# Kernel tuning notes

Measured on AMD Instinct MI355X. Metric: run time of the kernel, lower is better.

## Reference

```python
import jax, jax.numpy as jnp
import numpy as np

B = 16384          # batch
F_S = 26           # number of sparse features
F_D = 13           # number of dense features
V = 100000         # vocab per sparse feature
D = 64             # latent_dim


def setup_inputs() -> dict:
    key = jax.random.key(0)
    ks = jax.random.split(key, 8)
    sparse_idx = jax.random.randint(ks[0], (B, F_S), 0, V, dtype=jnp.int32)
    dense = jax.random.normal(ks[1], (B, F_D), dtype=jnp.float32)
    # Per-feature embedding tables, stacked: [F_S, V, *]
    emb_lin = jax.random.normal(ks[2], (F_S, V), dtype=jnp.float32) * 0.01      # linear_sparse (dim=1)
    emb_v = jax.random.normal(ks[3], (F_S, V, D), dtype=jnp.float32) * 0.01     # sparse_arch
    lin_dense_W = jax.random.normal(ks[4], (1, F_D), dtype=jnp.float32) * 0.1   # linear_dense
    lin_dense_b = jnp.zeros((1,), dtype=jnp.float32)
    dense_arch_W = jax.random.normal(ks[5], (D, F_D), dtype=jnp.float32) * 0.1  # dense_arch
    dense_arch_b = jnp.zeros((D,), dtype=jnp.float32)
    bias = jnp.zeros((1, 1), dtype=jnp.float32)
    return {
        "sparse_idx": sparse_idx, "dense": dense,
        "emb_lin": emb_lin, "emb_v": emb_v,
        "lin_dense_W": lin_dense_W, "lin_dense_b": lin_dense_b,
        "dense_arch_W": dense_arch_W, "dense_arch_b": dense_arch_b,
        "bias": bias,
    }


def reference(sparse_idx, dense, emb_lin, emb_v, lin_dense_W, lin_dense_b,
              dense_arch_W, dense_arch_b, bias):
    feat_ids = jnp.arange(F_S)[None, :]                       # [1, F_S]
    # ----- first-order term -----
    lin_d = dense @ lin_dense_W.T + lin_dense_b               # [B, 1]
    lin_s = emb_lin[feat_ids, sparse_idx]                     # [B, F_S] gather
    first = lin_d + lin_s.sum(axis=1, keepdims=True)          # [B, 1]
    # ----- second-order (FM) term -----
    v_d = dense @ dense_arch_W.T + dense_arch_b               # [B, D]
    v_s = emb_v[feat_ids, sparse_idx]                         # [B, F_S, D] gather
    vecs = jnp.concatenate([v_d[:, None, :], v_s], axis=1)    # [B, F_S+1, D]
    sum_of_square = jnp.square(vecs.sum(axis=1))              # [B, D]
    square_of_sum = jnp.square(vecs).sum(axis=1)              # [B, D]
    second = 0.5 * (sum_of_square - square_of_sum).sum(axis=1, keepdims=True)
    return first + second + bias                              # [B, 1]
```

## Files before the change

kernel.cpp:

```cpp
#include <hip/hip_runtime.h>

#define B   16384
#define F_S 26
#define F_D 13
#define V   100000
#define D   64

__global__ __launch_bounds__(256) void fm_kernel(
    const int*   __restrict__ sparse_idx,
    const float* __restrict__ dense,
    const float* __restrict__ emb_lin,
    const float* __restrict__ emb_v,
    const float* __restrict__ lin_dense_W,
    const float* __restrict__ lin_dense_b,
    const float* __restrict__ dense_arch_W,
    const float* __restrict__ dense_arch_b,
    const float* __restrict__ bias,
    float*       __restrict__ out)
{
    const int wave = threadIdx.x >> 6;
    const int lane = threadIdx.x & 63;
    const int row  = blockIdx.x * 4 + wave;

    int myidx = 0;
    if (lane < F_S) myidx = sparse_idx[row * F_S + lane];

    float dvals[F_D];
#pragma unroll
    for (int j = 0; j < F_D; ++j) dvals[j] = dense[row * F_D + j];

    float vd = dense_arch_b[lane];
#pragma unroll
    for (int j = 0; j < F_D; ++j)
        vd = fmaf(dense_arch_W[lane * F_D + j], dvals[j], vd);

    float S  = vd;
    float sq = vd * vd;

#pragma unroll
    for (int f = 0; f < F_S; ++f) {
        int idxf = __shfl(myidx, f);
        float val = emb_v[((size_t)f * V + (size_t)idxf) * D + lane];
        S  += val;
        sq  = fmaf(val, val, sq);
    }

    float part = 0.5f * (S * S - sq);
    if (lane < F_D) part = fmaf(dvals[lane], lin_dense_W[lane], part);
    if (lane < F_S) part += emb_lin[lane * V + myidx];

#pragma unroll
    for (int off = 32; off > 0; off >>= 1)
        part += __shfl_xor(part, off);

    if (lane == 0)
        out[row] = part + lin_dense_b[0] + bias[0];
}

extern "C" void kernel_launch(void* const* d_in, const int* in_sizes, int n_in,
                              void* d_out, int out_size, void* d_ws, size_t ws_size,
                              hipStream_t stream) {
    const int*   sparse_idx   = (const int*)  d_in[0];
    const float* dense        = (const float*)d_in[1];
    const float* emb_lin      = (const float*)d_in[2];
    const float* emb_v        = (const float*)d_in[3];
    const float* lin_dense_W  = (const float*)d_in[4];
    const float* lin_dense_b  = (const float*)d_in[5];
    const float* dense_arch_W = (const float*)d_in[6];
    const float* dense_arch_b = (const float*)d_in[7];
    const float* bias         = (const float*)d_in[8];
    float*       out          = (float*)d_out;

    fm_kernel<<<dim3(B / 4), dim3(256), 0, stream>>>(
        sparse_idx, dense, emb_lin, emb_v,
        lin_dense_W, lin_dense_b, dense_arch_W, dense_arch_b, bias, out);
}
```

Baseline: 743.1 us.

## Process four rows per wave with float4 embedding loads and LDS-staged indices

Result: no change. 743.8 us (+0.1%).

```diff
diff --git a/kernel.cpp b/kernel.cpp
--- a/kernel.cpp
+++ b/kernel.cpp
@@ -18,42 +18,71 @@
     const float* __restrict__ bias,
     float*       __restrict__ out)
 {
+    __shared__ int sidx[16 * F_S];
+
+    const int iblock = blockIdx.x * 16 * F_S;
+    sidx[threadIdx.x] = sparse_idx[iblock + threadIdx.x];
+    if (threadIdx.x < 16 * F_S - 256)
+        sidx[256 + threadIdx.x] = sparse_idx[iblock + 256 + threadIdx.x];
+    __syncthreads();
+
     const int wave = threadIdx.x >> 6;
     const int lane = threadIdx.x & 63;
-    const int row  = blockIdx.x * 4 + wave;
-
-    int myidx = 0;
-    if (lane < F_S) myidx = sparse_idx[row * F_S + lane];
+    const int sub  = lane >> 4;
+    const int t    = lane & 15;
+    const int rowl = wave * 4 + sub;
+    const int row  = blockIdx.x * 16 + rowl;
 
     float dvals[F_D];
 #pragma unroll
     for (int j = 0; j < F_D; ++j) dvals[j] = dense[row * F_D + j];
 
-    float vd = dense_arch_b[lane];
+    float4 S;
+    float  sq = 0.f;
+    {
+        float vd[4];
 #pragma unroll
-    for (int j = 0; j < F_D; ++j)
-        vd = fmaf(dense_arch_W[lane * F_D + j], dvals[j], vd);
+        for (int i = 0; i < 4; ++i) {
+            float acc = dense_arch_b[4 * t + i];
+#pragma unroll
+            for (int j = 0; j < F_D; ++j)
+                acc = fmaf(dense_arch_W[(4 * t + i) * F_D + j], dvals[j], acc);
+            vd[i] = acc;
+            sq = fmaf(acc, acc, sq);
+        }
+        S = make_float4(vd[0], vd[1], vd[2], vd[3]);
+    }
 
-    float S  = vd;
-    float sq = vd * vd;
+    const float4* __restrict__ emb_v4 = (const float4*)emb_v;
+#pragma unroll
+    for (int f = 0; f < F_S; ++f) {
+        int idxf = sidx[rowl * F_S + f];
+        float4 v = emb_v4[((size_t)f * V + (size_t)idxf) * 16 + t];
+        S.x += v.x; S.y += v.y; S.z += v.z; S.w += v.w;
+        sq = fmaf(v.x, v.x, sq);
+        sq = fmaf(v.y, v.y, sq);
+        sq = fmaf(v.z, v.z, sq);
+        sq = fmaf(v.w, v.w, sq);
+    }
+
+    float part = 0.5f * (S.x * S.x + S.y * S.y + S.z * S.z + S.w * S.w - sq);
+
+    {
+        int i0 = sidx[rowl * F_S + t];
+        part += emb_lin[(size_t)t * V + (size_t)i0];
+        if (t < F_S - 16) {
+            int i1 = sidx[rowl * F_S + t + 16];
+            part += emb_lin[(size_t)(t + 16) * V + (size_t)i1];
+        }
+    }
+    if (t < F_D)
+        part = fmaf(dense[row * F_D + t], lin_dense_W[t], part);
 
 #pragma unroll
-    for (int f = 0; f < F_S; ++f) {
-        int idxf = __shfl(myidx, f);
-        float val = emb_v[((size_t)f * V + (size_t)idxf) * D + lane];
-        S  += val;
-        sq  = fmaf(val, val, sq);
-    }
-
-    float part = 0.5f * (S * S - sq);
-    if (lane < F_D) part = fmaf(dvals[lane], lin_dense_W[lane], part);
-    if (lane < F_S) part += emb_lin[lane * V + myidx];
-
-#pragma unroll
-    for (int off = 32; off > 0; off >>= 1)
+    for (int off = 8; off > 0; off >>= 1)
         part += __shfl_xor(part, off);
 
-    if (lane == 0)
+    if (t == 0)
         out[row] = part + lin_dense_b[0] + bias[0];
 }
 
@@ -71,7 +100,7 @@
     const float* bias         = (const float*)d_in[8];
     float*       out          = (float*)d_out;
 
-    fm_kernel<<<dim3(B / 4), dim3(256), 0, stream>>>(
+    fm_kernel<<<dim3(B / 16), dim3(256), 0, stream>>>(
         sparse_idx, dense, emb_lin, emb_v,
         lin_dense_W, lin_dense_b, dense_arch_W, dense_arch_b, bias, out);
 }
```
